# Kernel tuning notes

Measured on AMD Instinct MI355X. Metric: run time of the kernel, lower is better.

## Reference

```python
import math
import jax, jax.numpy as jnp
import numpy as np

B, L, D = 2, 2048, 512
S, P = 4, 16  # n_orthogonal_sets, planes_per_set
TP = S * P


def setup_inputs() -> dict:
    key = jax.random.key(0)
    ks = jax.random.split(key, 12)
    sc = 0.02
    return {
        "x": jax.random.normal(ks[0], (B, L, D), dtype=jnp.float32),
        "set_weights": jnp.ones((S,), dtype=jnp.float32),
        "kw1": jax.random.normal(ks[1], (D, D), dtype=jnp.float32) * sc,
        "kb1": jnp.zeros((D,), dtype=jnp.float32),
        "kw2": jax.random.normal(ks[2], (D, TP), dtype=jnp.float32) * sc,
        "kb2": jnp.zeros((TP,), dtype=jnp.float32),
        "qw1": jax.random.normal(ks[3], (D, D), dtype=jnp.float32) * sc,
        "qb1": jnp.zeros((D,), dtype=jnp.float32),
        "qw2": jax.random.normal(ks[4], (D, TP), dtype=jnp.float32) * sc,
        "qb2": jnp.zeros((TP,), dtype=jnp.float32),
        "vw": jax.random.normal(ks[5], (D, D), dtype=jnp.float32) * sc,
        "vb": jnp.zeros((D,), dtype=jnp.float32),
        "ln_g": jnp.ones((D,), dtype=jnp.float32),
        "ln_b": jnp.zeros((D,), dtype=jnp.float32),
        "ow": jax.random.normal(ks[6], (D, D), dtype=jnp.float32) * sc,
        "ob": jnp.zeros((D,), dtype=jnp.float32),
    }


def reference(x, set_weights, kw1, kb1, kw2, kb2, qw1, qb1, qw2, qb2, vw, vb, ln_g, ln_b, ow, ob):
    b, l, d = x.shape
    # phase encoders: Linear -> GELU(exact) -> Linear, tanh * pi
    kp = jnp.tanh(jax.nn.gelu(x @ kw1 + kb1, approximate=False) @ kw2 + kb2) * math.pi
    qp = jnp.tanh(jax.nn.gelu(x @ qw1 + qb1, approximate=False) @ qw2 + qb2) * math.pi
    kp = kp.reshape(b, l, S, P)
    qp = qp.reshape(b, l, S, P)
    V = x @ vw + vb  # real values; phasor complex handled as (re, im)
    w = jax.nn.softmax(set_weights)
    total = jnp.zeros((b, l, d), dtype=x.dtype)
    for s in range(S):
        kc, ksn = jnp.cos(kp[:, :, s, :]), jnp.sin(kp[:, :, s, :])  # [b,l,P]
        # bound = e^{i kp} * V (V real); memory = cumsum over time
        Mre = jnp.cumsum(kc[..., None] * V[:, :, None, :], axis=1)  # [b,l,P,d]
        Mim = jnp.cumsum(ksn[..., None] * V[:, :, None, :], axis=1)
        # Re(memory * conj(e^{i qp})) summed over planes
        r = (jnp.einsum('blpd,blp->bld', Mre, jnp.cos(qp[:, :, s, :]))
             + jnp.einsum('blpd,blp->bld', Mim, jnp.sin(qp[:, :, s, :])))
        total = total + w[s] * r
    positions = jnp.arange(1, l + 1, dtype=x.dtype)
    norm = jnp.sqrt(positions * P)[None, :, None]
    y = total / norm
    mu = jnp.mean(y, axis=-1, keepdims=True)
    var = jnp.mean((y - mu) ** 2, axis=-1, keepdims=True)
    yn = (y - mu) / jnp.sqrt(var + 1e-5) * ln_g + ln_b
    return x + yn @ ow + ob
```

## Files before the change

### kernel.cpp

```cpp
#include <hip/hip_runtime.h>
#include <math.h>

constexpr int NB = 2;
constexpr int LQ = 2048;
constexpr int DD = 512;
constexpr int PPL = 16;
constexpr int TPP = 64;
constexpr int FF = 128;
constexpr int NC = 32;
constexpr int TC = 64;
constexpr float PI_F = 3.14159265358979323846f;

typedef __attribute__((ext_vector_type(4))) float f32x4;
typedef __attribute__((ext_vector_type(8))) short bf16x8;

static __device__ __forceinline__ unsigned short f2bf(float x) {
    union { float f; unsigned u; } v; v.f = x;
    unsigned r = v.u + 0x7fff + ((v.u >> 16) & 1);
    return (unsigned short)(r >> 16);
}
static __device__ __forceinline__ float bf2f(unsigned short u) {
    union { unsigned u; float f; } v; v.u = ((unsigned)u) << 16;
    return v.f;
}

__global__ __launch_bounds__(256) void cast_bf16(
    const float* __restrict__ x, unsigned short* __restrict__ o, int n)
{
    const int i = (blockIdx.x * 256 + threadIdx.x) * 8;
    if (i >= n) return;
    float4 a = *(const float4*)(x + i);
    float4 b = *(const float4*)(x + i + 4);
    ushort4 u0 = {f2bf(a.x), f2bf(a.y), f2bf(a.z), f2bf(a.w)};
    ushort4 u1 = {f2bf(b.x), f2bf(b.y), f2bf(b.z), f2bf(b.w)};
    *(ushort4*)(o + i) = u0;
    *(ushort4*)(o + i + 4) = u1;
}

__global__ __launch_bounds__(256) void wtrans_kernel(
    const float* __restrict__ w0, const float* __restrict__ w1,
    const float* __restrict__ w2, const float* __restrict__ w3,
    unsigned short* __restrict__ o0, unsigned short* __restrict__ o1,
    unsigned short* __restrict__ o2, unsigned short* __restrict__ o3,
    int K, int N)
{
    const float* W = (blockIdx.z == 0) ? w0 : (blockIdx.z == 1) ? w1 : (blockIdx.z == 2) ? w2 : w3;
    unsigned short* O = (blockIdx.z == 0) ? o0 : (blockIdx.z == 1) ? o1 : (blockIdx.z == 2) ? o2 : o3;
    __shared__ float t[32][33];
    const int tx = threadIdx.x & 31, ty = threadIdx.x >> 5;
    const int n0 = blockIdx.x * 32, k0 = blockIdx.y * 32;
#pragma unroll
    for (int i = 0; i < 4; ++i)
        t[ty + 8 * i][tx] = W[(size_t)(k0 + ty + 8 * i) * N + n0 + tx];
    __syncthreads();
#pragma unroll
    for (int i = 0; i < 4; ++i)
        O[(size_t)(n0 + ty + 8 * i) * K + k0 + tx] = f2bf(t[tx][ty + 8 * i]);
}

__global__ __launch_bounds__(256) void mgemm_fused(
    const unsigned short* __restrict__ A,
    const unsigned short* __restrict__ kw1t, const unsigned short* __restrict__ qw1t,
    const unsigned short* __restrict__ vwt,
    const float* __restrict__ kb1, const float* __restrict__ qb1, const float* __restrict__ vb,
    unsigned short* __restrict__ hkb, unsigned short* __restrict__ hqb,
    unsigned short* __restrict__ Vt)
{
    const int z = blockIdx.z;
    const unsigned short* Bt = (z == 0) ? kw1t : (z == 1) ? qw1t : vwt;
    const float* bias = (z == 0) ? kb1 : (z == 1) ? qb1 : vb;
    unsigned short* obf = (z == 0) ? hkb : (z == 1) ? hqb : Vt;
    const int K = DD, N = DD;

    __shared__ unsigned short As[128 * 72];
    __shared__ unsigned short Bs[64 * 72];
    const int tid = threadIdx.x;
    const int w = tid >> 6, lane = tid & 63, grp = lane >> 4, lid = lane & 15;
    const int wr = w >> 1, wc = w & 1;
    const int row0 = blockIdx.y * 128, col0 = blockIdx.x * 64;
    f32x4 acc[4][2];
#pragma unroll
    for (int m = 0; m < 4; ++m)
#pragma unroll
        for (int n = 0; n < 2; ++n) acc[m][n] = (f32x4)0.f;

    for (int k0 = 0; k0 < K; k0 += 64) {
        bf16x8 va[4], vbv[2];
#pragma unroll
        for (int i = 0; i < 4; ++i) {
            const int c = tid + i * 256;
            va[i] = *(const bf16x8*)(A + (size_t)(row0 + (c >> 3)) * K + k0 + (c & 7) * 8);
        }
#pragma unroll
        for (int i = 0; i < 2; ++i) {
            const int c = tid + i * 256;
            vbv[i] = *(const bf16x8*)(Bt + (size_t)(col0 + (c >> 3)) * K + k0 + (c & 7) * 8);
        }
        __syncthreads();
#pragma unroll
        for (int i = 0; i < 4; ++i) {
            const int c = tid + i * 256;
            *(bf16x8*)(As + (c >> 3) * 72 + (c & 7) * 8) = va[i];
        }
#pragma unroll
        for (int i = 0; i < 2; ++i) {
            const int c = tid + i * 256;
            *(bf16x8*)(Bs + (c >> 3) * 72 + (c & 7) * 8) = vbv[i];
        }
        __syncthreads();
#pragma unroll
        for (int kk = 0; kk < 2; ++kk) {
            bf16x8 af[4], bfr[2];
#pragma unroll
            for (int m = 0; m < 4; ++m)
                af[m] = *(const bf16x8*)(As + (wr * 64 + m * 16 + lid) * 72 + kk * 32 + grp * 8);
#pragma unroll
            for (int n = 0; n < 2; ++n)
                bfr[n] = *(const bf16x8*)(Bs + (wc * 32 + n * 16 + lid) * 72 + kk * 32 + grp * 8);
#pragma unroll
            for (int m = 0; m < 4; ++m)
#pragma unroll
                for (int n = 0; n < 2; ++n)
                    acc[m][n] = __builtin_amdgcn_mfma_f32_16x16x32_bf16(af[m], bfr[n], acc[m][n], 0, 0, 0);
        }
    }
#pragma unroll
    for (int m = 0; m < 4; ++m) {
#pragma unroll
        for (int n = 0; n < 2; ++n) {
            const int col = col0 + wc * 32 + n * 16 + lid;
            const float bc = bias[col];
            if (z == 2) {
                const int rowb = row0 + wr * 64 + m * 16 + grp * 4;
                const int b = rowb >> 11, l = rowb & (LQ - 1);
                const int c = l >> 6, t0 = l & 63;
                ushort4 u;
                u.x = f2bf(acc[m][n][0] + bc);
                u.y = f2bf(acc[m][n][1] + bc);
                u.z = f2bf(acc[m][n][2] + bc);
                u.w = f2bf(acc[m][n][3] + bc);
                *(ushort4*)(Vt + ((size_t)((b * NC + c) * DD) + col) * TC + t0) = u;
            } else {
#pragma unroll
                for (int r = 0; r < 4; ++r) {
                    const int row = row0 + wr * 64 + m * 16 + grp * 4 + r;
                    float v = acc[m][n][r] + bc;
                    v = 0.5f * v * (1.0f + erff(v * 0.70710678118654752f));
                    obf[(size_t)row * N + col] = f2bf(v);
                }
            }
        }
    }
}

__global__ __launch_bounds__(256) void phase_fused(
    const unsigned short* __restrict__ hkb, const unsigned short* __restrict__ hqb,
    const unsigned short* __restrict__ kw2t, const unsigned short* __restrict__ qw2t,
    const float* __restrict__ kb2, const float* __restrict__ qb2,
    const float* __restrict__ sw,
    unsigned short* __restrict__ CKb, unsigned short* __restrict__ CQb,
    unsigned short* __restrict__ CKt)
{
    const int isq = blockIdx.y;
    const unsigned short* A = isq ? hqb : hkb;
    const unsigned short* Bt = isq ? qw2t : kw2t;
    const float* b2 = isq ? qb2 : kb2;
    unsigned short* FROW = isq ? CQb : CKb;
    const int K = DD;

    __shared__ unsigned short As[64 * 72];
    __shared__ unsigned short Bs[64 * 72];
    const int tid = threadIdx.x;
    const int w = tid >> 6, lane = tid & 63, grp = lane >> 4, lid = lane & 15;
    const int row0 = blockIdx.x * 64;
    f32x4 acc[4];
#pragma unroll
    for (int n = 0; n < 4; ++n) acc[n] = (f32x4)0.f;

    for (int k0 = 0; k0 < K; k0 += 64) {
        bf16x8 va[2], vbv[2];
#pragma unroll
        for (int i = 0; i < 2; ++i) {
            const int c = tid + i * 256;
            va[i] = *(const bf16x8*)(A + (size_t)(row0 + (c >> 3)) * K + k0 + (c & 7) * 8);
            vbv[i] = *(const bf16x8*)(Bt + (size_t)(c >> 3) * K + k0 + (c & 7) * 8);
        }
        __syncthreads();
#pragma unroll
        for (int i = 0; i < 2; ++i) {
            const int c = tid + i * 256;
            *(bf16x8*)(As + (c >> 3) * 72 + (c & 7) * 8) = va[i];
            *(bf16x8*)(Bs + (c >> 3) * 72 + (c & 7) * 8) = vbv[i];
        }
        __syncthreads();
#pragma unroll
        for (int kk = 0; kk < 2; ++kk) {
            bf16x8 af, bfr[4];
            af = *(const bf16x8*)(As + (w * 16 + lid) * 72 + kk * 32 + grp * 8);
#pragma unroll
            for (int n = 0; n < 4; ++n)
                bfr[n] = *(const bf16x8*)(Bs + (n * 16 + lid) * 72 + kk * 32 + grp * 8);
#pragma unroll
            for (int n = 0; n < 4; ++n)
                acc[n] = __builtin_amdgcn_mfma_f32_16x16x32_bf16(af, bfr[n], acc[n], 0, 0, 0);
        }
    }
    float wsm[4] = {1.f, 1.f, 1.f, 1.f};
    if (isq) {
        float s0 = sw[0], s1 = sw[1], s2 = sw[2], s3 = sw[3];
        float mx = fmaxf(fmaxf(s0, s1), fmaxf(s2, s3));
        float e0 = expf(s0 - mx), e1 = expf(s1 - mx), e2 = expf(s2 - mx), e3 = expf(s3 - mx);
        float inv = 1.0f / (e0 + e1 + e2 + e3);
        wsm[0] = e0 * inv; wsm[1] = e1 * inv; wsm[2] = e2 * inv; wsm[3] = e3 * inv;
    }
#pragma unroll
    for (int n = 0; n < 4; ++n) {
        const int p = n * 16 + lid;
        const float bc = b2[p];
        const float wg = isq ? wsm[p >> 4] : 1.0f;
#pragma unroll
        for (int r = 0; r < 4; ++r) {
            const int row = row0 + w * 16 + grp * 4 + r;
            float u = acc[n][r] + bc;
            float ph = tanhf(u) * PI_F;
            float sp, cp;
            sincosf(ph, &sp, &cp);
            const unsigned short cb = f2bf(cp * wg), sb = f2bf(sp * wg);
            FROW[(size_t)row * FF + 2 * p + 0] = cb;
            FROW[(size_t)row * FF + 2 * p + 1] = sb;
            if (!isq) {
                const int b = row >> 11, l = row & (LQ - 1);
                const int c = l >> 6, t = l & 63;
                const size_t base = ((size_t)(b * NC + c) * FF) * TC;
                CKt[base + (size_t)(2 * p + 0) * TC + t] = cb;
                CKt[base + (size_t)(2 * p + 1) * TC + t] = sb;
            }
        }
    }
}

__global__ __launch_bounds__(256) void passA_mfma(
    const unsigned short* __restrict__ Vt, const unsigned short* __restrict__ CKt,
    unsigned short* __restrict__ Stp)
{
    const int tid = threadIdx.x;
    const int w = tid >> 6, lane = tid & 63, grp = lane >> 4, lid = lane & 15;
    const int dq = blockIdx.x, c = blockIdx.y, b = blockIdx.z;
    const int d0 = dq * 128 + w * 32;
    const size_t cb = (size_t)(b * NC + c);
    f32x4 acc[2][8];
#pragma unroll
    for (int md = 0; md < 2; ++md)
#pragma unroll
        for (int nf = 0; nf < 8; ++nf) acc[md][nf] = (f32x4)0.f;
#pragma unroll
    for (int kt = 0; kt < 2; ++kt) {
        bf16x8 av[2], bk[8];
#pragma unroll
        for (int md = 0; md < 2; ++md)
            av[md] = *(const bf16x8*)(Vt + (cb * DD + d0 + md * 16 + lid) * TC + kt * 32 + grp * 8);
#pragma unroll
        for (int nf = 0; nf < 8; ++nf)
            bk[nf] = *(const bf16x8*)(CKt + (cb * FF + nf * 16 + lid) * TC + kt * 32 + grp * 8);
#pragma unroll
        for (int md = 0; md < 2; ++md)
#pragma unroll
            for (int nf = 0; nf < 8; ++nf)
                acc[md][nf] = __builtin_amdgcn_mfma_f32_16x16x32_bf16(av[md], bk[nf], acc[md][nf], 0, 0, 0);
    }
#pragma unroll
    for (int md = 0; md < 2; ++md)
#pragma unroll
        for (int nf = 0; nf < 8; ++nf)
#pragma unroll
            for (int r = 0; r < 4; ++r) {
                const int d = d0 + md * 16 + grp * 4 + r;
                const int f = nf * 16 + lid;
                Stp[(cb * DD + d) * FF + f] = f2bf(acc[md][nf][r]);
            }
}

__global__ __launch_bounds__(256) void prefix_mfma(
    const unsigned short* __restrict__ Stp, unsigned short* __restrict__ Stb)
{
    const int gid = blockIdx.x * 256 + threadIdx.x;
    const int b = gid >> 16;
    const int df = gid & 65535;
    float run = 0.f;
#pragma unroll
    for (int c = 0; c < NC; ++c) {
        const size_t idx = ((size_t)(b * NC + c) << 16) + df;
        Stb[idx] = f2bf(run);
        run += bf2f(Stp[idx]);
    }
}

__global__ __launch_bounds__(128) void passC_mfma(
    const unsigned short* __restrict__ CQb, const unsigned short* __restrict__ CKb,
    const unsigned short* __restrict__ Vt, const unsigned short* __restrict__ Stb,
    float* __restrict__ R)
{
    __shared__ unsigned short P[64][72];
    const int tid = threadIdx.x;
    const int w = tid >> 6, lane = tid & 63, grp = lane >> 4, lid = lane & 15;
    const int dh = blockIdx.x, c = blockIdx.y, b = blockIdx.z;
    const size_t rowbase = (size_t)b * LQ + c * 64;
    const size_t cb = (size_t)(b * NC + c);
    f32x4 qk[2][4];
#pragma unroll
    for (int mi = 0; mi < 2; ++mi)
#pragma unroll
        for (int nt = 0; nt < 4; ++nt) qk[mi][nt] = (f32x4)0.f;
#pragma unroll
    for (int kf = 0; kf < 4; ++kf) {
        bf16x8 aq[2], bk[4];
#pragma unroll
        for (int mi = 0; mi < 2; ++mi)
            aq[mi] = *(const bf16x8*)(CQb + (rowbase + (2 * w + mi) * 16 + lid) * FF + kf * 32 + grp * 8);
#pragma unroll
        for (int nt = 0; nt < 4; ++nt)
            bk[nt] = *(const bf16x8*)(CKb + (rowbase + nt * 16 + lid) * FF + kf * 32 + grp * 8);
#pragma unroll
        for (int mi = 0; mi < 2; ++mi)
#pragma unroll
            for (int nt = 0; nt < 4; ++nt)
                qk[mi][nt] = __builtin_amdgcn_mfma_f32_16x16x32_bf16(aq[mi], bk[nt], qk[mi][nt], 0, 0, 0);
    }
#pragma unroll
    for (int mi = 0; mi < 2; ++mi)
#pragma unroll
        for (int nt = 0; nt < 4; ++nt)
#pragma unroll
            for (int r = 0; r < 4; ++r) {
                const int row = (2 * w + mi) * 16 + grp * 4 + r;
                const int col = nt * 16 + lid;
                P[row][col] = f2bf(col <= row ? qk[mi][nt][r] : 0.f);
            }
    __syncthreads();
    const int d0 = dh * 128 + w * 64;
    f32x4 racc[4][4];
#pragma unroll
    for (int ml = 0; ml < 4; ++ml)
#pragma unroll
        for (int nd = 0; nd < 4; ++nd) racc[ml][nd] = (f32x4)0.f;
#pragma unroll
    for (int kt = 0; kt < 2; ++kt) {
        bf16x8 ap[4], bv[4];
#pragma unroll
        for (int ml = 0; ml < 4; ++ml)
            ap[ml] = *(const bf16x8*)&P[ml * 16 + lid][kt * 32 + grp * 8];
#pragma unroll
        for (int nd = 0; nd < 4; ++nd)
            bv[nd] = *(const bf16x8*)(Vt + (cb * DD + d0 + nd * 16 + lid) * TC + kt * 32 + grp * 8);
#pragma unroll
        for (int ml = 0; ml < 4; ++ml)
#pragma unroll
            for (int nd = 0; nd < 4; ++nd)
                racc[ml][nd] = __builtin_amdgcn_mfma_f32_16x16x32_bf16(ap[ml], bv[nd], racc[ml][nd], 0, 0, 0);
    }
#pragma unroll
    for (int kf = 0; kf < 4; ++kf) {
        bf16x8 aq[4], bs[4];
#pragma unroll
        for (int ml = 0; ml < 4; ++ml)
            aq[ml] = *(const bf16x8*)(CQb + (rowbase + ml * 16 + lid) * FF + kf * 32 + grp * 8);
#pragma unroll
        for (int nd = 0; nd < 4; ++nd)
            bs[nd] = *(const bf16x8*)(Stb + (cb * DD + d0 + nd * 16 + lid) * FF + kf * 32 + grp * 8);
#pragma unroll
        for (int ml = 0; ml < 4; ++ml)
#pragma unroll
            for (int nd = 0; nd < 4; ++nd)
                racc[ml][nd] = __builtin_amdgcn_mfma_f32_16x16x32_bf16(aq[ml], bs[nd], racc[ml][nd], 0, 0, 0);
    }
#pragma unroll
    for (int ml = 0; ml < 4; ++ml)
#pragma unroll
        for (int nd = 0; nd < 4; ++nd)
#pragma unroll
            for (int r = 0; r < 4; ++r) {
                const int l = ml * 16 + grp * 4 + r;
                const int d = d0 + nd * 16 + lid;
                R[(rowbase + l) * DD + d] = racc[ml][nd][r];
            }
}

__global__ __launch_bounds__(256) void ln_kernel(
    const float* __restrict__ R, const float* __restrict__ g,
    const float* __restrict__ be, unsigned short* __restrict__ YN)
{
    const int row = blockIdx.x;
    const int l = row & (LQ - 1);
    const int tid = threadIdx.x;
    const float pscale = rsqrtf((float)((l + 1) * PPL));
    float y0 = R[(size_t)row * DD + tid] * pscale;
    float y1 = R[(size_t)row * DD + 256 + tid] * pscale;
    float s = y0 + y1;
    float q = y0 * y0 + y1 * y1;
#pragma unroll
    for (int off = 32; off >= 1; off >>= 1) {
        s += __shfl_xor(s, off, 64);
        q += __shfl_xor(q, off, 64);
    }
    __shared__ float rs[4], rq[4];
    const int wid = tid >> 6, lane = tid & 63;
    if (lane == 0) { rs[wid] = s; rq[wid] = q; }
    __syncthreads();
    const float ts = rs[0] + rs[1] + rs[2] + rs[3];
    const float tq = rq[0] + rq[1] + rq[2] + rq[3];
    const float mu = ts * (1.0f / DD);
    float var = tq * (1.0f / DD) - mu * mu;
    const float rstd = rsqrtf(var + 1e-5f);
    YN[(size_t)row * DD + tid] = f2bf((y0 - mu) * rstd * g[tid] + be[tid]);
    YN[(size_t)row * DD + 256 + tid] = f2bf((y1 - mu) * rstd * g[tid + 256] + be[tid + 256]);
}

__global__ __launch_bounds__(256) void mgemm_out(
    const unsigned short* __restrict__ A, const unsigned short* __restrict__ Bt,
    const float* __restrict__ bias, const float* __restrict__ resid,
    float* __restrict__ out)
{
    const int K = DD, N = DD;
    __shared__ unsigned short As[64 * 72];
    __shared__ unsigned short Bs[64 * 72];
    const int tid = threadIdx.x;
    const int w = tid >> 6, lane = tid & 63, grp = lane >> 4, lid = lane & 15;
    const int wr = w >> 1, wc = w & 1;
    const int row0 = blockIdx.y * 64, col0 = blockIdx.x * 64;
    f32x4 acc[2][2];
#pragma unroll
    for (int m = 0; m < 2; ++m)
#pragma unroll
        for (int n = 0; n < 2; ++n) acc[m][n] = (f32x4)0.f;

    for (int k0 = 0; k0 < K; k0 += 64) {
        bf16x8 va[2], vbv[2];
#pragma unroll
        for (int i = 0; i < 2; ++i) {
            const int c = tid + i * 256;
            va[i] = *(const bf16x8*)(A + (size_t)(row0 + (c >> 3)) * K + k0 + (c & 7) * 8);
            vbv[i] = *(const bf16x8*)(Bt + (size_t)(col0 + (c >> 3)) * K + k0 + (c & 7) * 8);
        }
        __syncthreads();
#pragma unroll
        for (int i = 0; i < 2; ++i) {
            const int c = tid + i * 256;
            *(bf16x8*)(As + (c >> 3) * 72 + (c & 7) * 8) = va[i];
            *(bf16x8*)(Bs + (c >> 3) * 72 + (c & 7) * 8) = vbv[i];
        }
        __syncthreads();
#pragma unroll
        for (int kk = 0; kk < 2; ++kk) {
            bf16x8 af[2], bfr[2];
#pragma unroll
            for (int m = 0; m < 2; ++m)
                af[m] = *(const bf16x8*)(As + (wr * 32 + m * 16 + lid) * 72 + kk * 32 + grp * 8);
#pragma unroll
            for (int n = 0; n < 2; ++n)
                bfr[n] = *(const bf16x8*)(Bs + (wc * 32 + n * 16 + lid) * 72 + kk * 32 + grp * 8);
#pragma unroll
            for (int m = 0; m < 2; ++m)
#pragma unroll
                for (int n = 0; n < 2; ++n)
                    acc[m][n] = __builtin_amdgcn_mfma_f32_16x16x32_bf16(af[m], bfr[n], acc[m][n], 0, 0, 0);
        }
    }
#pragma unroll
    for (int m = 0; m < 2; ++m) {
#pragma unroll
        for (int n = 0; n < 2; ++n) {
            const int col = col0 + wc * 32 + n * 16 + lid;
            const float bc = bias[col];
#pragma unroll
            for (int r = 0; r < 4; ++r) {
                const int row = row0 + wr * 32 + m * 16 + grp * 4 + r;
                out[(size_t)row * N + col] = acc[m][n][r] + bc + resid[(size_t)row * N + col];
            }
        }
    }
}

extern "C" void kernel_launch(void* const* d_in, const int* in_sizes, int n_in,
                              void* d_out, int out_size, void* d_ws, size_t ws_size,
                              hipStream_t stream)
{
    const float* x   = (const float*)d_in[0];
    const float* sw  = (const float*)d_in[1];
    const float* kw1 = (const float*)d_in[2];
    const float* kb1 = (const float*)d_in[3];
    const float* kw2 = (const float*)d_in[4];
    const float* kb2 = (const float*)d_in[5];
    const float* qw1 = (const float*)d_in[6];
    const float* qb1 = (const float*)d_in[7];
    const float* qw2 = (const float*)d_in[8];
    const float* qb2 = (const float*)d_in[9];
    const float* vw  = (const float*)d_in[10];
    const float* vb  = (const float*)d_in[11];
    const float* lng = (const float*)d_in[12];
    const float* lnb = (const float*)d_in[13];
    const float* ow  = (const float*)d_in[14];
    const float* ob  = (const float*)d_in[15];
    float* out = (float*)d_out;

    const size_t MR = (size_t)NB * LQ;
    float* ws = (float*)d_ws;
    float* Rb = ws;
    unsigned short* xb   = (unsigned short*)(Rb + MR * DD);
    unsigned short* hkb  = xb + MR * DD;
    unsigned short* hqb  = hkb + MR * DD;
    unsigned short* YNb  = hqb + MR * DD;
    unsigned short* Vt   = YNb + MR * DD;
    unsigned short* CQb  = Vt + MR * DD;
    unsigned short* CKb  = CQb + MR * FF;
    unsigned short* CKt  = CKb + MR * FF;
    unsigned short* Stp  = CKt + MR * FF;
    unsigned short* Stb  = Stp + (size_t)NB * NC * DD * FF;
    unsigned short* kw1t = Stb + (size_t)NB * NC * DD * FF;
    unsigned short* qw1t = kw1t + (size_t)DD * DD;
    unsigned short* vwt  = qw1t + (size_t)DD * DD;
    unsigned short* owt  = vwt + (size_t)DD * DD;
    unsigned short* kw2t = owt + (size_t)DD * DD;
    unsigned short* qw2t = kw2t + (size_t)TPP * DD;

    const dim3 blk(256);
    hipLaunchKernelGGL(cast_bf16, dim3((unsigned)(MR * DD / 2048)), blk, 0, stream, x, xb, (int)(MR * DD));
    hipLaunchKernelGGL(wtrans_kernel, dim3(16, 16, 4), blk, 0, stream,
                       kw1, qw1, vw, ow, kw1t, qw1t, vwt, owt, DD, DD);
    hipLaunchKernelGGL(wtrans_kernel, dim3(2, 16, 2), blk, 0, stream,
                       kw2, qw2, kw2, qw2, kw2t, qw2t, kw2t, qw2t, DD, TPP);

    hipLaunchKernelGGL(mgemm_fused, dim3(DD / 64, MR / 128, 3), blk, 0, stream,
                       xb, kw1t, qw1t, vwt, kb1, qb1, vb, hkb, hqb, Vt);
    hipLaunchKernelGGL(phase_fused, dim3(MR / 64, 2), blk, 0, stream,
                       hkb, hqb, kw2t, qw2t, kb2, qb2, sw, CKb, CQb, CKt);

    hipLaunchKernelGGL(passA_mfma, dim3(4, NC, NB), blk, 0, stream, Vt, CKt, Stp);
    hipLaunchKernelGGL(prefix_mfma, dim3((NB * DD * FF) / 256), blk, 0, stream, Stp, Stb);
    hipLaunchKernelGGL(passC_mfma, dim3(4, NC, NB), dim3(128), 0, stream, CQb, CKb, Vt, Stb, Rb);
    hipLaunchKernelGGL(ln_kernel, dim3((unsigned)MR), blk, 0, stream, Rb, lng, lnb, YNb);
    hipLaunchKernelGGL(mgemm_out, dim3(DD / 64, MR / 64), blk, 0, stream, YNb, owt, ob, x, out);
}
```

Measured before the change: 154.2 us.

## Merge prep kernels into one launch and fuse layernorm into output GEMM

Combines the x cast and the two weight-transpose launches into a single prep kernel dispatched by block index. It also removes the standalone layernorm kernel: the output GEMM now computes per-row mean and rstd from the fp32 result rows and normalizes and casts to bf16 while loading the A tile. This saves two launches and the bf16 YN round trip through memory. In exchange, each of the 8 column blocks re-reads the fp32 rows, once for statistics and again per k-tile.

```diff
diff --git a/kernel.cpp b/kernel.cpp
--- a/kernel.cpp
+++ b/kernel.cpp
@@ -24,31 +24,48 @@
     return v.f;
 }
 
-__global__ __launch_bounds__(256) void cast_bf16(
-    const float* __restrict__ x, unsigned short* __restrict__ o, int n)
-{
-    const int i = (blockIdx.x * 256 + threadIdx.x) * 8;
-    if (i >= n) return;
-    float4 a = *(const float4*)(x + i);
-    float4 b = *(const float4*)(x + i + 4);
-    ushort4 u0 = {f2bf(a.x), f2bf(a.y), f2bf(a.z), f2bf(a.w)};
-    ushort4 u1 = {f2bf(b.x), f2bf(b.y), f2bf(b.z), f2bf(b.w)};
-    *(ushort4*)(o + i) = u0;
-    *(ushort4*)(o + i + 4) = u1;
-}
-
-__global__ __launch_bounds__(256) void wtrans_kernel(
-    const float* __restrict__ w0, const float* __restrict__ w1,
-    const float* __restrict__ w2, const float* __restrict__ w3,
-    unsigned short* __restrict__ o0, unsigned short* __restrict__ o1,
-    unsigned short* __restrict__ o2, unsigned short* __restrict__ o3,
-    int K, int N)
-{
-    const float* W = (blockIdx.z == 0) ? w0 : (blockIdx.z == 1) ? w1 : (blockIdx.z == 2) ? w2 : w3;
-    unsigned short* O = (blockIdx.z == 0) ? o0 : (blockIdx.z == 1) ? o1 : (blockIdx.z == 2) ? o2 : o3;
+__global__ __launch_bounds__(256) void prep_kernel(
+    const float* __restrict__ x,
+    const float* __restrict__ kw1, const float* __restrict__ qw1,
+    const float* __restrict__ vw, const float* __restrict__ ow,
+    const float* __restrict__ kw2, const float* __restrict__ qw2,
+    unsigned short* __restrict__ xb,
+    unsigned short* __restrict__ kw1t, unsigned short* __restrict__ qw1t,
+    unsigned short* __restrict__ vwt, unsigned short* __restrict__ owt,
+    unsigned short* __restrict__ kw2t, unsigned short* __restrict__ qw2t)
+{
     __shared__ float t[32][33];
-    const int tx = threadIdx.x & 31, ty = threadIdx.x >> 5;
-    const int n0 = blockIdx.x * 32, k0 = blockIdx.y * 32;
+    const int id = blockIdx.x;
+    const int tid = threadIdx.x;
+    if (id < 1024) {
+        const int i = id * 2048 + tid * 8;
+        float4 a = *(const float4*)(x + i);
+        float4 b = *(const float4*)(x + i + 4);
+        ushort4 u0 = {f2bf(a.x), f2bf(a.y), f2bf(a.z), f2bf(a.w)};
+        ushort4 u1 = {f2bf(b.x), f2bf(b.y), f2bf(b.z), f2bf(b.w)};
+        *(ushort4*)(xb + i) = u0;
+        *(ushort4*)(xb + i + 4) = u1;
+        return;
+    }
+    const float* W;
+    unsigned short* O;
+    int K, N, n0, k0;
+    if (id < 2048) {
+        const int rid = id - 1024;
+        const int mat = rid >> 8, rem = rid & 255;
+        W = (mat == 0) ? kw1 : (mat == 1) ? qw1 : (mat == 2) ? vw : ow;
+        O = (mat == 0) ? kw1t : (mat == 1) ? qw1t : (mat == 2) ? vwt : owt;
+        K = DD; N = DD;
+        n0 = (rem & 15) * 32; k0 = (rem >> 4) * 32;
+    } else {
+        const int rid = id - 2048;
+        const int mat = rid >> 5, rem = rid & 31;
+        W = mat ? qw2 : kw2;
+        O = mat ? qw2t : kw2t;
+        K = DD; N = TPP;
+        n0 = (rem & 1) * 32; k0 = (rem >> 1) * 32;
+    }
+    const int tx = tid & 31, ty = tid >> 5;
 #pragma unroll
     for (int i = 0; i < 4; ++i)
         t[ty + 8 * i][tx] = W[(size_t)(k0 + ty + 8 * i) * N + n0 + tx];
@@ -385,48 +402,48 @@
             }
 }
 
-__global__ __launch_bounds__(256) void ln_kernel(
-    const float* __restrict__ R, const float* __restrict__ g,
-    const float* __restrict__ be, unsigned short* __restrict__ YN)
-{
-    const int row = blockIdx.x;
-    const int l = row & (LQ - 1);
-    const int tid = threadIdx.x;
-    const float pscale = rsqrtf((float)((l + 1) * PPL));
-    float y0 = R[(size_t)row * DD + tid] * pscale;
-    float y1 = R[(size_t)row * DD + 256 + tid] * pscale;
-    float s = y0 + y1;
-    float q = y0 * y0 + y1 * y1;
-#pragma unroll
-    for (int off = 32; off >= 1; off >>= 1) {
-        s += __shfl_xor(s, off, 64);
-        q += __shfl_xor(q, off, 64);
-    }
-    __shared__ float rs[4], rq[4];
-    const int wid = tid >> 6, lane = tid & 63;
-    if (lane == 0) { rs[wid] = s; rq[wid] = q; }
-    __syncthreads();
-    const float ts = rs[0] + rs[1] + rs[2] + rs[3];
-    const float tq = rq[0] + rq[1] + rq[2] + rq[3];
-    const float mu = ts * (1.0f / DD);
-    float var = tq * (1.0f / DD) - mu * mu;
-    const float rstd = rsqrtf(var + 1e-5f);
-    YN[(size_t)row * DD + tid] = f2bf((y0 - mu) * rstd * g[tid] + be[tid]);
-    YN[(size_t)row * DD + 256 + tid] = f2bf((y1 - mu) * rstd * g[tid + 256] + be[tid + 256]);
-}
-
-__global__ __launch_bounds__(256) void mgemm_out(
-    const unsigned short* __restrict__ A, const unsigned short* __restrict__ Bt,
+__global__ __launch_bounds__(256) void ln_out_gemm(
+    const float* __restrict__ Rb, const float* __restrict__ g,
+    const float* __restrict__ be, const unsigned short* __restrict__ Bt,
     const float* __restrict__ bias, const float* __restrict__ resid,
     float* __restrict__ out)
 {
     const int K = DD, N = DD;
     __shared__ unsigned short As[64 * 72];
     __shared__ unsigned short Bs[64 * 72];
+    __shared__ float smu[64], srs[64], sps[64], sg[512], sbe[512];
     const int tid = threadIdx.x;
     const int w = tid >> 6, lane = tid & 63, grp = lane >> 4, lid = lane & 15;
     const int wr = w >> 1, wc = w & 1;
     const int row0 = blockIdx.y * 64, col0 = blockIdx.x * 64;
+
+    sg[tid] = g[tid]; sg[tid + 256] = g[tid + 256];
+    sbe[tid] = be[tid]; sbe[tid + 256] = be[tid + 256];
+
+    {
+        const int rr = tid >> 2, seg = tid & 3;
+        const float* rp = Rb + (size_t)(row0 + rr) * DD + seg * 128;
+        float s = 0.f, q = 0.f;
+#pragma unroll
+        for (int j = 0; j < 32; ++j) {
+            float4 v = *(const float4*)(rp + j * 4);
+            s += v.x + v.y + v.z + v.w;
+            q += v.x * v.x + v.y * v.y + v.z * v.z + v.w * v.w;
+        }
+        s += __shfl_xor(s, 1, 64); q += __shfl_xor(q, 1, 64);
+        s += __shfl_xor(s, 2, 64); q += __shfl_xor(q, 2, 64);
+        if (seg == 0) {
+            const int l = (row0 + rr) & (LQ - 1);
+            const float ps = rsqrtf((float)((l + 1) * PPL));
+            const float mu = s * (1.0f / DD) * ps;
+            const float ey2 = q * (1.0f / DD) * ps * ps;
+            smu[rr] = mu;
+            srs[rr] = rsqrtf(ey2 - mu * mu + 1e-5f);
+            sps[rr] = ps;
+        }
+    }
+    __syncthreads();
+
     f32x4 acc[2][2];
 #pragma unroll
     for (int m = 0; m < 2; ++m)
@@ -434,18 +451,34 @@
         for (int n = 0; n < 2; ++n) acc[m][n] = (f32x4)0.f;
 
     for (int k0 = 0; k0 < K; k0 += 64) {
-        bf16x8 va[2], vbv[2];
+        ushort4 ua[2][2];
+        bf16x8 vbv[2];
 #pragma unroll
         for (int i = 0; i < 2; ++i) {
             const int c = tid + i * 256;
-            va[i] = *(const bf16x8*)(A + (size_t)(row0 + (c >> 3)) * K + k0 + (c & 7) * 8);
-            vbv[i] = *(const bf16x8*)(Bt + (size_t)(col0 + (c >> 3)) * K + k0 + (c & 7) * 8);
+            const int r = c >> 3, kb = (c & 7) * 8;
+            const float mu = smu[r], rs = srs[r], ps = sps[r];
+            const float* rp = Rb + (size_t)(row0 + r) * DD + k0 + kb;
+            float4 a0 = *(const float4*)rp;
+            float4 a1 = *(const float4*)(rp + 4);
+            const float* gg = sg + k0 + kb;
+            const float* bb = sbe + k0 + kb;
+            ua[i][0].x = f2bf((a0.x * ps - mu) * rs * gg[0] + bb[0]);
+            ua[i][0].y = f2bf((a0.y * ps - mu) * rs * gg[1] + bb[1]);
+            ua[i][0].z = f2bf((a0.z * ps - mu) * rs * gg[2] + bb[2]);
+            ua[i][0].w = f2bf((a0.w * ps - mu) * rs * gg[3] + bb[3]);
+            ua[i][1].x = f2bf((a1.x * ps - mu) * rs * gg[4] + bb[4]);
+            ua[i][1].y = f2bf((a1.y * ps - mu) * rs * gg[5] + bb[5]);
+            ua[i][1].z = f2bf((a1.z * ps - mu) * rs * gg[6] + bb[6]);
+            ua[i][1].w = f2bf((a1.w * ps - mu) * rs * gg[7] + bb[7]);
+            vbv[i] = *(const bf16x8*)(Bt + (size_t)(col0 + r) * K + k0 + kb);
         }
         __syncthreads();
 #pragma unroll
         for (int i = 0; i < 2; ++i) {
             const int c = tid + i * 256;
-            *(bf16x8*)(As + (c >> 3) * 72 + (c & 7) * 8) = va[i];
+            *(ushort4*)(As + (c >> 3) * 72 + (c & 7) * 8) = ua[i][0];
+            *(ushort4*)(As + (c >> 3) * 72 + (c & 7) * 8 + 4) = ua[i][1];
             *(bf16x8*)(Bs + (c >> 3) * 72 + (c & 7) * 8) = vbv[i];
         }
         __syncthreads();
@@ -508,8 +541,7 @@
     unsigned short* xb   = (unsigned short*)(Rb + MR * DD);
     unsigned short* hkb  = xb + MR * DD;
     unsigned short* hqb  = hkb + MR * DD;
-    unsigned short* YNb  = hqb + MR * DD;
-    unsigned short* Vt   = YNb + MR * DD;
+    unsigned short* Vt   = hqb + MR * DD;
     unsigned short* CQb  = Vt + MR * DD;
     unsigned short* CKb  = CQb + MR * FF;
     unsigned short* CKt  = CKb + MR * FF;
@@ -523,20 +555,16 @@
     unsigned short* qw2t = kw2t + (size_t)TPP * DD;
 
     const dim3 blk(256);
-    hipLaunchKernelGGL(cast_bf16, dim3((unsigned)(MR * DD / 2048)), blk, 0, stream, x, xb, (int)(MR * DD));
-    hipLaunchKernelGGL(wtrans_kernel, dim3(16, 16, 4), blk, 0, stream,
-                       kw1, qw1, vw, ow, kw1t, qw1t, vwt, owt, DD, DD);
-    hipLaunchKernelGGL(wtrans_kernel, dim3(2, 16, 2), blk, 0, stream,
-                       kw2, qw2, kw2, qw2, kw2t, qw2t, kw2t, qw2t, DD, TPP);
-
+    hipLaunchKernelGGL(prep_kernel, dim3(2112), blk, 0, stream,
+                       x, kw1, qw1, vw, ow, kw2, qw2,
+                       xb, kw1t, qw1t, vwt, owt, kw2t, qw2t);
     hipLaunchKernelGGL(mgemm_fused, dim3(DD / 64, MR / 128, 3), blk, 0, stream,
                        xb, kw1t, qw1t, vwt, kb1, qb1, vb, hkb, hqb, Vt);
     hipLaunchKernelGGL(phase_fused, dim3(MR / 64, 2), blk, 0, stream,
                        hkb, hqb, kw2t, qw2t, kb2, qb2, sw, CKb, CQb, CKt);
-
     hipLaunchKernelGGL(passA_mfma, dim3(4, NC, NB), blk, 0, stream, Vt, CKt, Stp);
     hipLaunchKernelGGL(prefix_mfma, dim3((NB * DD * FF) / 256), blk, 0, stream, Stp, Stb);
     hipLaunchKernelGGL(passC_mfma, dim3(4, NC, NB), dim3(128), 0, stream, CQb, CKb, Vt, Stb, Rb);
-    hipLaunchKernelGGL(ln_kernel, dim3((unsigned)MR), blk, 0, stream, Rb, lng, lnb, YNb);
-    hipLaunchKernelGGL(mgemm_out, dim3(DD / 64, MR / 64), blk, 0, stream, YNb, owt, ob, x, out);
-}
+    hipLaunchKernelGGL(ln_out_gemm, dim3(DD / 64, MR / 64), blk, 0, stream,
+                       Rb, lng, lnb, owt, ob, x, out);
+}
```

New measurement: 159.9 us. 3.7% more time.
